# Performance work log

Measured on AMD Instinct MI355X. Metric: run time of the kernel, lower is better.

The kernel has to match this reference:

```python
import jax, jax.numpy as jnp
import numpy as np
import math

MU = 5; ETA = 1.0; ITERS = 3
SIGMA_C = 1.0; SIGMA_S = 1.6 * SIGMA_C
SIGMA_M = 3.0; RHO = 0.99; TAU = 0.7
MAX_T = int(math.floor(3 * SIGMA_C))  # 3
MAX_S = int(math.floor(3 * SIGMA_M))  # 9
DELTA = 1.0
B, C, X, Y = 4, 1, 512, 512


def _gpdf(v, sig):
    return math.exp(-v * v / (2.0 * sig * sig)) / (math.sqrt(2.0 * math.pi) * sig)


def _sobel(img):
    k = jnp.array([[-1., -2., -1.], [0., 0., 0.], [1., 2., 1.]], dtype=img.dtype)
    kern = jnp.stack([k, k.T])[:, None]  # [2,1,3,3] OIHW
    return jax.lax.conv_general_dilated(img, kern, (1, 1), [(1, 1), (1, 1)],
                                        dimension_numbers=('NCHW', 'OIHW', 'NCHW'))


def _gather_flat(arr, idx):
    # arr [b,c,x,y], idx int [b,x,y] flattened spatial index (px*Y+py)
    b, c, x, y = arr.shape
    flat = arr.reshape(b, c, x * y)
    idxb = jnp.broadcast_to(idx.reshape(b, 1, x * y), (b, c, x * y))
    return jnp.take_along_axis(flat, idxb, axis=2).reshape(b, c, x, y)


def _safe_norm(v):
    m = jnp.linalg.norm(v, axis=1, keepdims=True)
    return v / jnp.where(m == 0, 1.0, m)


def _etf(images):
    b, c, x, y = images.shape
    sob = _sobel(images)                                   # [b,2,x,y]
    mag = jnp.linalg.norm(sob, axis=1, keepdims=True)      # [b,1,x,y]
    mag = mag / jnp.max(mag)
    mag_p = jnp.pad(mag, ((0, 0), (0, 0), (MU, MU), (MU, MU)))
    sobel_X = mag[:, None]                                 # [b,1,1,x,y]
    tang = _safe_norm(jnp.stack([-sob[:, 1], sob[:, 0]], axis=1))
    K = 2 * MU + 1
    for _ in range(ITERS):
        for ori in ('V', 'H'):
            tang_p = jnp.pad(tang, ((0, 0), (0, 0), (MU, MU), (MU, MU)))
            tang_X = tang[:, None]                         # [b,1,2,x,y]
            if ori == 'V':
                tang_Y = jnp.stack([tang_p[:, :, i:i + x, MU:MU + y] for i in range(K)], axis=1)
                sobel_Y = jnp.stack([mag_p[:, :, i:i + x, MU:MU + y] for i in range(K)], axis=1)
            else:
                tang_Y = jnp.stack([tang_p[:, :, MU:MU + x, i:i + y] for i in range(K)], axis=1)
                sobel_Y = jnp.stack([mag_p[:, :, MU:MU + x, i:i + y] for i in range(K)], axis=1)
            # weight: magnitude term * direction term / 2
            w = (jnp.tanh(ETA * (sobel_Y - sobel_X)) + 1.0) \
                * jnp.sum(tang_X * tang_Y, axis=2, keepdims=True) * 0.5
            tang = _safe_norm(jnp.sum(tang_Y * w, axis=1))
    return tang


def _dog(images, etf):
    b, c, x, y = images.shape
    xi, yi = jnp.meshgrid(jnp.arange(x, dtype=images.dtype),
                          jnp.arange(y, dtype=images.dtype), indexing='ij')
    idx0 = jnp.broadcast_to(jnp.stack([xi, yi])[None], (b, 2, x, y))
    per = jnp.stack([-etf[:, 1], etf[:, 0]], axis=1)       # perpendicular to flow
    dog = jnp.zeros_like(images)
    tw = 0.0
    for t in range(-MAX_T, MAX_T + 1):
        pts = idx0 + DELTA * per * t
        px = jnp.round(jnp.clip(pts[:, 0], 0, x - 1)).astype(jnp.int32)
        py = jnp.round(jnp.clip(pts[:, 1], 0, y - 1)).astype(jnp.int32)
        il = _gather_flat(images, px * y + py)
        gw = _gpdf(t, SIGMA_C) - RHO * _gpdf(t, SIGMA_S)
        tw += gw
        dog = dog + il * gw
    return dog / tw


def _fdog_float(images):
    b, c, x, y = images.shape
    etf = _etf(images)
    dog = _dog(images, etf)
    fdog = jnp.zeros_like(images)
    tw = 0.0
    xi, yi = jnp.meshgrid(jnp.arange(x, dtype=jnp.int32),
                          jnp.arange(y, dtype=jnp.int32), indexing='ij')
    for s_dir in (-1, 1):
        px = jnp.broadcast_to(xi[None], (b, x, y))
        py = jnp.broadcast_to(yi[None], (b, x, y))
        for s in range(0 if s_dir == 1 else 1, MAX_S + 1):
            if s != 0:
                p_etf = _gather_flat(etf, px * y + py)     # flow at current points
                fx = px.astype(images.dtype) + DELTA * p_etf[:, 0] * s_dir
                fy = py.astype(images.dtype) + DELTA * p_etf[:, 1] * s_dir
                px = jnp.round(jnp.clip(fx, 0, x - 1)).astype(jnp.int32)
                py = jnp.round(jnp.clip(fy, 0, y - 1)).astype(jnp.int32)
            f_s = _gather_flat(dog, px * y + py)
            gw = _gpdf(s, SIGMA_M)
            tw += gw
            fdog = fdog + f_s * gw
    return fdog / tw


def setup_inputs() -> dict:
    key = jax.random.key(0)
    images = jax.random.uniform(key, (B, C, X, Y), dtype=jnp.float32)
    return {"images": images}


def reference(images):
    fdog = _fdog_float(images)
    edges = ~((fdog < 0) & (1.0 + jnp.tanh(fdog) < TAU))
    return edges.astype(jnp.int32)
```

## Files before the change

### kernel.cpp

```cpp
#include <hip/hip_runtime.h>
#include <math.h>

#pragma clang fp contract(off)

#define BN 4
#define SX 512
#define SY 512
#define NPIX (BN * SX * SY)
#define MU 5
#define MB (1024 * 1024)
#define NBLOCKS 4096

struct DogW  { float g[7];  float tw; };
struct FdogW { float g[10]; float tw; };

__device__ __forceinline__ float fast_tanh_f32(float dF) {
    double d = (double)dF;
    double y = fabs(d);
    double t = expm1(2.0 * y);
    double r = t / (t + 2.0);
    if (y > 350.0) r = 1.0;
    return (float)copysign(r, d);
}

__device__ __forceinline__ int clampi(int v, int lo, int hi) {
    return v < lo ? lo : (v > hi ? hi : v);
}

__global__ __launch_bounds__(256) void k_sobel(const float* __restrict__ img,
                                               float* __restrict__ mag,
                                               float2* __restrict__ tang,
                                               float* __restrict__ partial) {
#pragma clang fp contract(off)
    int yi = blockIdx.x * blockDim.x + threadIdx.x;
    int xi = blockIdx.y;
    int b  = blockIdx.z;
    size_t base = (size_t)b * SX * SY;

    int xm = clampi(xi - 1, 0, SX - 1), xp = clampi(xi + 1, 0, SX - 1);
    int ym = clampi(yi - 1, 0, SY - 1), yp = clampi(yi + 1, 0, SY - 1);
    float l00 = img[base + (size_t)xm * SY + ym];
    float l01 = img[base + (size_t)xm * SY + yi];
    float l02 = img[base + (size_t)xm * SY + yp];
    float l10 = img[base + (size_t)xi * SY + ym];
    float l12 = img[base + (size_t)xi * SY + yp];
    float l20 = img[base + (size_t)xp * SY + ym];
    float l21 = img[base + (size_t)xp * SY + yi];
    float l22 = img[base + (size_t)xp * SY + yp];
    bool vxm = (xi - 1) >= 0, vxp = (xi + 1) < SX;
    bool vym = (yi - 1) >= 0, vyp = (yi + 1) < SY;
    float v00 = (vxm && vym) ? l00 : 0.0f;
    float v01 = (vxm       ) ? l01 : 0.0f;
    float v02 = (vxm && vyp) ? l02 : 0.0f;
    float v10 = (       vym) ? l10 : 0.0f;
    float v12 = (       vyp) ? l12 : 0.0f;
    float v20 = (vxp && vym) ? l20 : 0.0f;
    float v21 = (vxp       ) ? l21 : 0.0f;
    float v22 = (vxp && vyp) ? l22 : 0.0f;

    float s0 = (-1.0f * v00);
    s0 = s0 + (-2.0f * v01);
    s0 = s0 + (-1.0f * v02);
    s0 = s0 + ( 1.0f * v20);
    s0 = s0 + ( 2.0f * v21);
    s0 = s0 + ( 1.0f * v22);
    float s1 = (-1.0f * v00);
    s1 = s1 + ( 1.0f * v02);
    s1 = s1 + (-2.0f * v10);
    s1 = s1 + ( 2.0f * v12);
    s1 = s1 + (-1.0f * v20);
    s1 = s1 + ( 1.0f * v22);

    float m = sqrtf((s0 * s0) + (s1 * s1));
    size_t idx = base + (size_t)xi * SY + yi;
    mag[idx] = m;

    float tx = -s1, ty = s0;
    float n = sqrtf((tx * tx) + (ty * ty));
    float d = (n == 0.0f) ? 1.0f : n;
    tang[idx] = make_float2(tx / d, ty / d);

    float wm = m;
    for (int off = 32; off > 0; off >>= 1) wm = fmaxf(wm, __shfl_down(wm, off, 64));
    __shared__ float red[4];
    int lane = threadIdx.x & 63;
    int wid  = threadIdx.x >> 6;
    if (lane == 0) red[wid] = wm;
    __syncthreads();
    if (threadIdx.x == 0) {
        float bm = fmaxf(fmaxf(red[0], red[1]), fmaxf(red[2], red[3]));
        int bid = blockIdx.x + gridDim.x * (blockIdx.y + gridDim.y * blockIdx.z);
        partial[bid] = bm;
    }
}

__global__ void k_reduce(const float* __restrict__ partial, unsigned int* __restrict__ maxbits) {
    float m = 0.0f;
    for (int i = threadIdx.x; i < NBLOCKS; i += 256) m = fmaxf(m, partial[i]);
    for (int off = 32; off > 0; off >>= 1) m = fmaxf(m, __shfl_down(m, off, 64));
    __shared__ float red[4];
    int lane = threadIdx.x & 63;
    int wid  = threadIdx.x >> 6;
    if (lane == 0) red[wid] = m;
    __syncthreads();
    if (threadIdx.x == 0)
        *maxbits = __float_as_uint(fmaxf(fmaxf(red[0], red[1]), fmaxf(red[2], red[3])));
}

__global__ __launch_bounds__(256) void k_tanh(const float* __restrict__ mag,
                                              const unsigned int* __restrict__ maxbits,
                                              float* __restrict__ TV, float* __restrict__ TH) {
#pragma clang fp contract(off)
    int yi = blockIdx.x * blockDim.x + threadIdx.x;
    int xi = blockIdx.y;
    int b  = blockIdx.z;
    size_t base = (size_t)b * SX * SY;
    size_t idx  = base + (size_t)xi * SY + yi;
    float mx = __uint_as_float(*maxbits);

    float mv[5], mh[5];
#pragma unroll
    for (int k = 1; k <= 5; ++k)
        mv[k - 1] = mag[base + (size_t)clampi(xi + k, 0, SX - 1) * SY + yi];
#pragma unroll
    for (int k = 1; k <= 5; ++k)
        mh[k - 1] = mag[base + (size_t)xi * SY + clampi(yi + k, 0, SY - 1)];
    float cm = mag[idx] / mx;

#pragma unroll
    for (int k = 1; k <= 5; ++k) {
        if (xi + k < SX)
            TV[(size_t)(k - 1) * NPIX + idx] = fast_tanh_f32((mv[k - 1] / mx) - cm);
    }
#pragma unroll
    for (int k = 1; k <= 5; ++k) {
        if (yi + k < SY)
            TH[(size_t)(k - 1) * NPIX + idx] = fast_tanh_f32((mh[k - 1] / mx) - cm);
    }
}

__global__ __launch_bounds__(256) void k_etf_v(const float2* __restrict__ tsrc,
                                               float2* __restrict__ tdst,
                                               const float* __restrict__ TV) {
#pragma clang fp contract(off)
    int yi = blockIdx.x * blockDim.x + threadIdx.x;
    int xi = blockIdx.y;
    int b  = blockIdx.z;
    size_t base = (size_t)b * SX * SY;
    size_t idx  = base + (size_t)xi * SY + yi;

    float2 nt[11];
    float  tv[11];
#pragma unroll
    for (int k = -MU; k <= MU; ++k) {
        int nxc = clampi(xi + k, 0, SX - 1);
        nt[k + MU] = tsrc[base + (size_t)nxc * SY + yi];
        if (k > 0)      tv[k + MU] = TV[(size_t)(k - 1) * NPIX + idx];
        else if (k < 0) tv[k + MU] = TV[(size_t)(-k - 1) * NPIX + base + (size_t)nxc * SY + yi];
        else            tv[k + MU] = 0.0f;
    }
    float2 ct = nt[MU];

    float sx = 0.0f, sy = 0.0f;
#pragma unroll
    for (int k = -MU; k <= MU; ++k) {
        bool valid = ((unsigned)(xi + k)) < (unsigned)SX;
        float2 v = nt[k + MU];
        float vx = valid ? v.x : 0.0f;
        float vy = valid ? v.y : 0.0f;
        float th;
        if (k > 0)      th = valid ?  tv[k + MU] : 0.0f;
        else if (k < 0) th = valid ? -tv[k + MU] : 0.0f;
        else            th = 0.0f;
        float dot = (ct.x * vx) + (ct.y * vy);
        float w   = ((th + 1.0f) * dot) * 0.5f;
        sx = sx + (vx * w);
        sy = sy + (vy * w);
    }
    float n = sqrtf((sx * sx) + (sy * sy));
    float d = (n == 0.0f) ? 1.0f : n;
    tdst[idx] = make_float2(sx / d, sy / d);
}

__global__ __launch_bounds__(256) void k_etf_h(const float2* __restrict__ tsrc,
                                               float2* __restrict__ tdst,
                                               const float* __restrict__ TH) {
#pragma clang fp contract(off)
    int yi = blockIdx.x * blockDim.x + threadIdx.x;
    int xi = blockIdx.y;
    int b  = blockIdx.z;
    size_t base = (size_t)b * SX * SY;
    size_t rowb = base + (size_t)xi * SY;
    size_t idx  = rowb + yi;

    float2 nt[11];
    float  tv[11];
#pragma unroll
    for (int k = -MU; k <= MU; ++k) {
        int nyc = clampi(yi + k, 0, SY - 1);
        nt[k + MU] = tsrc[rowb + nyc];
        if (k > 0)      tv[k + MU] = TH[(size_t)(k - 1) * NPIX + idx];
        else if (k < 0) tv[k + MU] = TH[(size_t)(-k - 1) * NPIX + rowb + nyc];
        else            tv[k + MU] = 0.0f;
    }
    float2 ct = nt[MU];

    float sx = 0.0f, sy = 0.0f;
#pragma unroll
    for (int k = -MU; k <= MU; ++k) {
        bool valid = ((unsigned)(yi + k)) < (unsigned)SY;
        float2 v = nt[k + MU];
        float vx = valid ? v.x : 0.0f;
        float vy = valid ? v.y : 0.0f;
        float th;
        if (k > 0)      th = valid ?  tv[k + MU] : 0.0f;
        else if (k < 0) th = valid ? -tv[k + MU] : 0.0f;
        else            th = 0.0f;
        float dot = (ct.x * vx) + (ct.y * vy);
        float w   = ((th + 1.0f) * dot) * 0.5f;
        sx = sx + (vx * w);
        sy = sy + (vy * w);
    }
    float n = sqrtf((sx * sx) + (sy * sy));
    float d = (n == 0.0f) ? 1.0f : n;
    tdst[idx] = make_float2(sx / d, sy / d);
}

__global__ __launch_bounds__(256) void k_dog(const float* __restrict__ img,
                                             const float2* __restrict__ etf,
                                             float* __restrict__ dog, DogW w) {
#pragma clang fp contract(off)
    int yi = blockIdx.x * blockDim.x + threadIdx.x;
    int xi = blockIdx.y;
    int b  = blockIdx.z;
    size_t base = (size_t)b * SX * SY;
    size_t idx  = base + (size_t)xi * SY + yi;

    float2 e = etf[idx];
    float perx = -e.y;
    float pery =  e.x;
    float xf = (float)xi, yf = (float)yi;

    float il[7];
#pragma unroll
    for (int t = -3; t <= 3; ++t) {
        float tf  = (float)t;
        float ptx = xf + (perx * tf);
        float pty = yf + (pery * tf);
        int px = (int)rintf(fminf(fmaxf(ptx, 0.0f), (float)(SX - 1)));
        int py = (int)rintf(fminf(fmaxf(pty, 0.0f), (float)(SY - 1)));
        il[t + 3] = img[base + (size_t)px * SY + py];
    }
    float acc = 0.0f;
#pragma unroll
    for (int t = -3; t <= 3; ++t) acc = acc + (il[t + 3] * w.g[t + 3]);
    dog[idx] = acc / w.tw;
}

__global__ __launch_bounds__(256) void k_fdog(const float* __restrict__ dog,
                                              const float2* __restrict__ etf,
                                              int* __restrict__ out, FdogW w) {
#pragma clang fp contract(off)
    int yi = blockIdx.x * blockDim.x + threadIdx.x;
    int xi = blockIdx.y;
    int b  = blockIdx.z;
    size_t base = (size_t)b * SX * SY;
    size_t idx  = base + (size_t)xi * SY + yi;

    float d1[9];
    float d2[10];
    float2 e0 = etf[idx];
    float2 e1 = e0, e2 = e0;
    int p1x = xi, p1y = yi;
    int p2x = xi, p2y = yi;
    d2[0] = dog[idx];

#pragma unroll
    for (int s = 1; s <= 9; ++s) {
        float fx1 = (float)p1x + (e1.x * -1.0f);
        float fy1 = (float)p1y + (e1.y * -1.0f);
        p1x = (int)rintf(fminf(fmaxf(fx1, 0.0f), (float)(SX - 1)));
        p1y = (int)rintf(fminf(fmaxf(fy1, 0.0f), (float)(SY - 1)));
        size_t i1 = base + (size_t)p1x * SY + p1y;
        float fx2 = (float)p2x + (e2.x * 1.0f);
        float fy2 = (float)p2y + (e2.y * 1.0f);
        p2x = (int)rintf(fminf(fmaxf(fx2, 0.0f), (float)(SX - 1)));
        p2y = (int)rintf(fminf(fmaxf(fy2, 0.0f), (float)(SY - 1)));
        size_t i2 = base + (size_t)p2x * SY + p2y;

        d1[s - 1] = dog[i1];
        d2[s]     = dog[i2];
        if (s < 9) {
            e1 = etf[i1];
            e2 = etf[i2];
        }
    }

    float acc = 0.0f;
#pragma unroll
    for (int s = 1; s <= 9; ++s) acc = acc + (d1[s - 1] * w.g[s]);
    acc = acc + (d2[0] * w.g[0]);
#pragma unroll
    for (int s = 1; s <= 9; ++s) acc = acc + (d2[s] * w.g[s]);

    float fv = acc / w.tw;
    float th = 1.0f + fast_tanh_f32(fv);
    out[idx] = ((fv < 0.0f) && (th < 0.7f)) ? 0 : 1;
}

static double gpdf(double v, double sig) {
    return exp(-(v * v) / (2.0 * sig * sig)) / (sqrt(2.0 * M_PI) * sig);
}

extern "C" void kernel_launch(void* const* d_in, const int* in_sizes, int n_in,
                              void* d_out, int out_size, void* d_ws, size_t ws_size,
                              hipStream_t stream) {
    const float* img = (const float*)d_in[0];
    int* out = (int*)d_out;
    char* ws = (char*)d_ws;

    float*  mag = (float*)(ws);
    float2* tA  = (float2*)(ws + (size_t)4  * MB);
    float2* tB  = (float2*)(ws + (size_t)12 * MB);
    float*  TV  = (float*)(ws + (size_t)20 * MB);
    float*  TH  = (float*)(ws + (size_t)40 * MB);
    float*  dog = (float*)(ws + (size_t)60 * MB);
    float*        partial = (float*)(ws + (size_t)64 * MB);
    unsigned int* maxbits = (unsigned int*)(ws + (size_t)64 * MB + NBLOCKS * sizeof(float));

    DogW dw;
    {
        double tw = 0.0;
        for (int t = -3; t <= 3; ++t) {
            double g = gpdf((double)t, 1.0) - 0.99 * gpdf((double)t, 1.6);
            dw.g[t + 3] = (float)g;
            tw += g;
        }
        dw.tw = (float)tw;
    }
    FdogW fw;
    {
        for (int s = 0; s <= 9; ++s) fw.g[s] = (float)gpdf((double)s, 3.0);
        double tw = 0.0;
        for (int s = 1; s <= 9; ++s) tw += gpdf((double)s, 3.0);
        for (int s = 0; s <= 9; ++s) tw += gpdf((double)s, 3.0);
        fw.tw = (float)tw;
    }

    dim3 blk(256, 1, 1);
    dim3 grd(SY / 256, SX, BN);

    k_sobel<<<grd, blk, 0, stream>>>(img, mag, tA, partial);
    k_reduce<<<1, 256, 0, stream>>>(partial, maxbits);
    k_tanh<<<grd, blk, 0, stream>>>(mag, maxbits, TV, TH);

    float2* src = tA;
    float2* dst = tB;
    for (int it = 0; it < 3; ++it) {
        k_etf_v<<<grd, blk, 0, stream>>>(src, dst, TV);
        { float2* t = src; src = dst; dst = t; }
        k_etf_h<<<grd, blk, 0, stream>>>(src, dst, TH);
        { float2* t = src; src = dst; dst = t; }
    }
    k_dog<<<grd, blk, 0, stream>>>(img, src, dog, dw);
    k_fdog<<<grd, blk, 0, stream>>>(dog, src, out, fw);
}
```

Measured before the change: 201.5 us.

## Fuse DoG into final ETF horizontal pass and process two pixels per thread

Each ETF kernel now covers a full 512-wide row per block, with every thread computing two pixels, so the grid shrinks to one block per row. The last horizontal ETF pass also computes the perpendicular DoG sample in the same kernel, which removes the separate k_dog launch and its re-read of the ETF field. The cost is doubled register arrays per thread, which may lower occupancy, and half as many blocks.

```diff
diff --git a/kernel.cpp b/kernel.cpp
--- a/kernel.cpp
+++ b/kernel.cpp
@@ -139,122 +139,181 @@
     }
 }
 
+struct EtfAcc { float sx, sy; };
+
 __global__ __launch_bounds__(256) void k_etf_v(const float2* __restrict__ tsrc,
                                                float2* __restrict__ tdst,
                                                const float* __restrict__ TV) {
 #pragma clang fp contract(off)
-    int yi = blockIdx.x * blockDim.x + threadIdx.x;
-    int xi = blockIdx.y;
-    int b  = blockIdx.z;
-    size_t base = (size_t)b * SX * SY;
-    size_t idx  = base + (size_t)xi * SY + yi;
-
-    float2 nt[11];
-    float  tv[11];
-#pragma unroll
-    for (int k = -MU; k <= MU; ++k) {
-        int nxc = clampi(xi + k, 0, SX - 1);
-        nt[k + MU] = tsrc[base + (size_t)nxc * SY + yi];
-        if (k > 0)      tv[k + MU] = TV[(size_t)(k - 1) * NPIX + idx];
-        else if (k < 0) tv[k + MU] = TV[(size_t)(-k - 1) * NPIX + base + (size_t)nxc * SY + yi];
-        else            tv[k + MU] = 0.0f;
-    }
-    float2 ct = nt[MU];
-
-    float sx = 0.0f, sy = 0.0f;
-#pragma unroll
-    for (int k = -MU; k <= MU; ++k) {
-        bool valid = ((unsigned)(xi + k)) < (unsigned)SX;
-        float2 v = nt[k + MU];
-        float vx = valid ? v.x : 0.0f;
-        float vy = valid ? v.y : 0.0f;
-        float th;
-        if (k > 0)      th = valid ?  tv[k + MU] : 0.0f;
-        else if (k < 0) th = valid ? -tv[k + MU] : 0.0f;
-        else            th = 0.0f;
-        float dot = (ct.x * vx) + (ct.y * vy);
-        float w   = ((th + 1.0f) * dot) * 0.5f;
-        sx = sx + (vx * w);
-        sy = sy + (vy * w);
-    }
-    float n = sqrtf((sx * sx) + (sy * sy));
-    float d = (n == 0.0f) ? 1.0f : n;
-    tdst[idx] = make_float2(sx / d, sy / d);
+    int tid = (int)threadIdx.x;
+    int xi = blockIdx.y;
+    int b  = blockIdx.z;
+    size_t base = (size_t)b * SX * SY;
+
+    float2 nt2[2][11];
+    float  tv2[2][11];
+#pragma unroll
+    for (int p = 0; p < 2; ++p) {
+        int yi = tid + p * 256;
+        size_t idx = base + (size_t)xi * SY + yi;
+#pragma unroll
+        for (int k = -MU; k <= MU; ++k) {
+            int nxc = clampi(xi + k, 0, SX - 1);
+            nt2[p][k + MU] = tsrc[base + (size_t)nxc * SY + yi];
+            if (k > 0)      tv2[p][k + MU] = TV[(size_t)(k - 1) * NPIX + idx];
+            else if (k < 0) tv2[p][k + MU] = TV[(size_t)(-k - 1) * NPIX + base + (size_t)nxc * SY + yi];
+            else            tv2[p][k + MU] = 0.0f;
+        }
+    }
+#pragma unroll
+    for (int p = 0; p < 2; ++p) {
+        int yi = tid + p * 256;
+        size_t idx = base + (size_t)xi * SY + yi;
+        float2 ct = nt2[p][MU];
+        float sx = 0.0f, sy = 0.0f;
+#pragma unroll
+        for (int k = -MU; k <= MU; ++k) {
+            bool valid = ((unsigned)(xi + k)) < (unsigned)SX;
+            float2 v = nt2[p][k + MU];
+            float vx = valid ? v.x : 0.0f;
+            float vy = valid ? v.y : 0.0f;
+            float th;
+            if (k > 0)      th = valid ?  tv2[p][k + MU] : 0.0f;
+            else if (k < 0) th = valid ? -tv2[p][k + MU] : 0.0f;
+            else            th = 0.0f;
+            float dot = (ct.x * vx) + (ct.y * vy);
+            float w   = ((th + 1.0f) * dot) * 0.5f;
+            sx = sx + (vx * w);
+            sy = sy + (vy * w);
+        }
+        float n = sqrtf((sx * sx) + (sy * sy));
+        float d = (n == 0.0f) ? 1.0f : n;
+        tdst[idx] = make_float2(sx / d, sy / d);
+    }
 }
 
 __global__ __launch_bounds__(256) void k_etf_h(const float2* __restrict__ tsrc,
                                                float2* __restrict__ tdst,
                                                const float* __restrict__ TH) {
 #pragma clang fp contract(off)
-    int yi = blockIdx.x * blockDim.x + threadIdx.x;
+    int tid = (int)threadIdx.x;
     int xi = blockIdx.y;
     int b  = blockIdx.z;
     size_t base = (size_t)b * SX * SY;
     size_t rowb = base + (size_t)xi * SY;
-    size_t idx  = rowb + yi;
-
-    float2 nt[11];
-    float  tv[11];
-#pragma unroll
-    for (int k = -MU; k <= MU; ++k) {
-        int nyc = clampi(yi + k, 0, SY - 1);
-        nt[k + MU] = tsrc[rowb + nyc];
-        if (k > 0)      tv[k + MU] = TH[(size_t)(k - 1) * NPIX + idx];
-        else if (k < 0) tv[k + MU] = TH[(size_t)(-k - 1) * NPIX + rowb + nyc];
-        else            tv[k + MU] = 0.0f;
-    }
-    float2 ct = nt[MU];
-
-    float sx = 0.0f, sy = 0.0f;
-#pragma unroll
-    for (int k = -MU; k <= MU; ++k) {
-        bool valid = ((unsigned)(yi + k)) < (unsigned)SY;
-        float2 v = nt[k + MU];
-        float vx = valid ? v.x : 0.0f;
-        float vy = valid ? v.y : 0.0f;
-        float th;
-        if (k > 0)      th = valid ?  tv[k + MU] : 0.0f;
-        else if (k < 0) th = valid ? -tv[k + MU] : 0.0f;
-        else            th = 0.0f;
-        float dot = (ct.x * vx) + (ct.y * vy);
-        float w   = ((th + 1.0f) * dot) * 0.5f;
-        sx = sx + (vx * w);
-        sy = sy + (vy * w);
-    }
-    float n = sqrtf((sx * sx) + (sy * sy));
-    float d = (n == 0.0f) ? 1.0f : n;
-    tdst[idx] = make_float2(sx / d, sy / d);
-}
-
-__global__ __launch_bounds__(256) void k_dog(const float* __restrict__ img,
-                                             const float2* __restrict__ etf,
-                                             float* __restrict__ dog, DogW w) {
-#pragma clang fp contract(off)
-    int yi = blockIdx.x * blockDim.x + threadIdx.x;
-    int xi = blockIdx.y;
-    int b  = blockIdx.z;
-    size_t base = (size_t)b * SX * SY;
-    size_t idx  = base + (size_t)xi * SY + yi;
-
-    float2 e = etf[idx];
-    float perx = -e.y;
-    float pery =  e.x;
-    float xf = (float)xi, yf = (float)yi;
-
-    float il[7];
-#pragma unroll
-    for (int t = -3; t <= 3; ++t) {
-        float tf  = (float)t;
-        float ptx = xf + (perx * tf);
-        float pty = yf + (pery * tf);
-        int px = (int)rintf(fminf(fmaxf(ptx, 0.0f), (float)(SX - 1)));
-        int py = (int)rintf(fminf(fmaxf(pty, 0.0f), (float)(SY - 1)));
-        il[t + 3] = img[base + (size_t)px * SY + py];
-    }
-    float acc = 0.0f;
-#pragma unroll
-    for (int t = -3; t <= 3; ++t) acc = acc + (il[t + 3] * w.g[t + 3]);
-    dog[idx] = acc / w.tw;
+
+    float2 nt2[2][11];
+    float  tv2[2][11];
+#pragma unroll
+    for (int p = 0; p < 2; ++p) {
+        int yi = tid + p * 256;
+        size_t idx = rowb + yi;
+#pragma unroll
+        for (int k = -MU; k <= MU; ++k) {
+            int nyc = clampi(yi + k, 0, SY - 1);
+            nt2[p][k + MU] = tsrc[rowb + nyc];
+            if (k > 0)      tv2[p][k + MU] = TH[(size_t)(k - 1) * NPIX + idx];
+            else if (k < 0) tv2[p][k + MU] = TH[(size_t)(-k - 1) * NPIX + rowb + nyc];
+            else            tv2[p][k + MU] = 0.0f;
+        }
+    }
+#pragma unroll
+    for (int p = 0; p < 2; ++p) {
+        int yi = tid + p * 256;
+        size_t idx = rowb + yi;
+        float2 ct = nt2[p][MU];
+        float sx = 0.0f, sy = 0.0f;
+#pragma unroll
+        for (int k = -MU; k <= MU; ++k) {
+            bool valid = ((unsigned)(yi + k)) < (unsigned)SY;
+            float2 v = nt2[p][k + MU];
+            float vx = valid ? v.x : 0.0f;
+            float vy = valid ? v.y : 0.0f;
+            float th;
+            if (k > 0)      th = valid ?  tv2[p][k + MU] : 0.0f;
+            else if (k < 0) th = valid ? -tv2[p][k + MU] : 0.0f;
+            else            th = 0.0f;
+            float dot = (ct.x * vx) + (ct.y * vy);
+            float w   = ((th + 1.0f) * dot) * 0.5f;
+            sx = sx + (vx * w);
+            sy = sy + (vy * w);
+        }
+        float n = sqrtf((sx * sx) + (sy * sy));
+        float d = (n == 0.0f) ? 1.0f : n;
+        tdst[idx] = make_float2(sx / d, sy / d);
+    }
+}
+
+__global__ __launch_bounds__(256) void k_etf_h_dog(const float2* __restrict__ tsrc,
+                                                   float2* __restrict__ tdst,
+                                                   const float* __restrict__ TH,
+                                                   const float* __restrict__ img,
+                                                   float* __restrict__ dogbuf, DogW dw) {
+#pragma clang fp contract(off)
+    int tid = (int)threadIdx.x;
+    int xi = blockIdx.y;
+    int b  = blockIdx.z;
+    size_t base = (size_t)b * SX * SY;
+    size_t rowb = base + (size_t)xi * SY;
+
+    float2 nt2[2][11];
+    float  tv2[2][11];
+#pragma unroll
+    for (int p = 0; p < 2; ++p) {
+        int yi = tid + p * 256;
+        size_t idx = rowb + yi;
+#pragma unroll
+        for (int k = -MU; k <= MU; ++k) {
+            int nyc = clampi(yi + k, 0, SY - 1);
+            nt2[p][k + MU] = tsrc[rowb + nyc];
+            if (k > 0)      tv2[p][k + MU] = TH[(size_t)(k - 1) * NPIX + idx];
+            else if (k < 0) tv2[p][k + MU] = TH[(size_t)(-k - 1) * NPIX + rowb + nyc];
+            else            tv2[p][k + MU] = 0.0f;
+        }
+    }
+#pragma unroll
+    for (int p = 0; p < 2; ++p) {
+        int yi = tid + p * 256;
+        size_t idx = rowb + yi;
+        float2 ct = nt2[p][MU];
+        float sx = 0.0f, sy = 0.0f;
+#pragma unroll
+        for (int k = -MU; k <= MU; ++k) {
+            bool valid = ((unsigned)(yi + k)) < (unsigned)SY;
+            float2 v = nt2[p][k + MU];
+            float vx = valid ? v.x : 0.0f;
+            float vy = valid ? v.y : 0.0f;
+            float th;
+            if (k > 0)      th = valid ?  tv2[p][k + MU] : 0.0f;
+            else if (k < 0) th = valid ? -tv2[p][k + MU] : 0.0f;
+            else            th = 0.0f;
+            float dot = (ct.x * vx) + (ct.y * vy);
+            float w   = ((th + 1.0f) * dot) * 0.5f;
+            sx = sx + (vx * w);
+            sy = sy + (vy * w);
+        }
+        float n = sqrtf((sx * sx) + (sy * sy));
+        float d = (n == 0.0f) ? 1.0f : n;
+        float ex = sx / d, ey = sy / d;
+        tdst[idx] = make_float2(ex, ey);
+
+        float perx = -ey, pery = ex;
+        float xf = (float)xi, yf = (float)yi;
+        float il[7];
+#pragma unroll
+        for (int t = -3; t <= 3; ++t) {
+            float tf  = (float)t;
+            float ptx = xf + (perx * tf);
+            float pty = yf + (pery * tf);
+            int px = (int)rintf(fminf(fmaxf(ptx, 0.0f), (float)(SX - 1)));
+            int py = (int)rintf(fminf(fmaxf(pty, 0.0f), (float)(SY - 1)));
+            il[t + 3] = img[base + (size_t)px * SY + py];
+        }
+        float acc = 0.0f;
+#pragma unroll
+        for (int t = -3; t <= 3; ++t) acc = acc + (il[t + 3] * dw.g[t + 3]);
+        dogbuf[idx] = acc / dw.tw;
+    }
 }
 
 __global__ __launch_bounds__(256) void k_fdog(const float* __restrict__ dog,
@@ -349,19 +408,18 @@
 
     dim3 blk(256, 1, 1);
     dim3 grd(SY / 256, SX, BN);
+    dim3 rgrd(1, SX, BN);
 
     k_sobel<<<grd, blk, 0, stream>>>(img, mag, tA, partial);
     k_reduce<<<1, 256, 0, stream>>>(partial, maxbits);
     k_tanh<<<grd, blk, 0, stream>>>(mag, maxbits, TV, TH);
 
-    float2* src = tA;
-    float2* dst = tB;
-    for (int it = 0; it < 3; ++it) {
-        k_etf_v<<<grd, blk, 0, stream>>>(src, dst, TV);
-        { float2* t = src; src = dst; dst = t; }
-        k_etf_h<<<grd, blk, 0, stream>>>(src, dst, TH);
-        { float2* t = src; src = dst; dst = t; }
-    }
-    k_dog<<<grd, blk, 0, stream>>>(img, src, dog, dw);
-    k_fdog<<<grd, blk, 0, stream>>>(dog, src, out, fw);
-}
+    k_etf_v<<<rgrd, blk, 0, stream>>>(tA, tB, TV);
+    k_etf_h<<<rgrd, blk, 0, stream>>>(tB, tA, TH);
+    k_etf_v<<<rgrd, blk, 0, stream>>>(tA, tB, TV);
+    k_etf_h<<<rgrd, blk, 0, stream>>>(tB, tA, TH);
+    k_etf_v<<<rgrd, blk, 0, stream>>>(tA, tB, TV);
+    k_etf_h_dog<<<rgrd, blk, 0, stream>>>(tB, tA, TH, img, dog, dw);
+
+    k_fdog<<<grd, blk, 0, stream>>>(dog, tA, out, fw);
+}
```

Result: slower. 226.0 us (+12.2%).
